# Optimization experiments

Hardware: AMD Instinct MI355X
Metric: run time of the kernel (lower is better)

The kernel has to match this reference:

```python
import jax, jax.numpy as jnp
import numpy as np

B, T, N = 128, 1024, 64


def setup_inputs() -> dict:
    key = jax.random.key(0)
    k1, k2, k3, k4, k5 = jax.random.split(key, 5)
    potentials = jax.random.normal(k1, (B, T, N), dtype=jnp.float32)
    tags = jax.random.randint(k2, (B, T), 0, N, dtype=jnp.int32)
    # valid lengths in [T//2, T] so every sequence has at least one step
    sequence_length = jax.random.randint(k3, (B,), T // 2, T + 1, dtype=jnp.int32)
    chain_kernel = jax.random.normal(k4, (N, N), dtype=jnp.float32)
    sample_weight = jax.random.uniform(k5, (B,), dtype=jnp.float32)
    return {
        "potentials": potentials,
        "tags": tags,
        "sequence_length": sequence_length,
        "chain_kernel": chain_kernel,
        "sample_weight": sample_weight,
    }


def _crf_sequence_score(potentials, tags, sequence_length, chain_kernel):
    # potentials: [B,T,N], tags: [B,T] int, chain_kernel: [N,N]
    Bx, Tx, Nx = potentials.shape
    t_idx = jnp.arange(Tx)
    mask = (t_idx[None, :] < sequence_length[:, None]).astype(potentials.dtype)  # [B,T]
    # unary score: potentials at the gold tag per step
    unary = jnp.take_along_axis(potentials, tags[..., None].astype(jnp.int32), axis=2)[..., 0]  # [B,T]
    unary_score = jnp.sum(unary * mask, axis=1)  # [B]
    # binary score: transitions tag[t] -> tag[t+1], valid if t+1 < seq_len
    trans_sc = chain_kernel[tags[:, :-1], tags[:, 1:]]  # [B,T-1]
    binary_score = jnp.sum(trans_sc * mask[:, 1:], axis=1)  # [B]
    return unary_score + binary_score


def _crf_log_norm(potentials, sequence_length, chain_kernel):
    # forward algorithm with lax.scan over time
    Bx, Tx, Nx = potentials.shape
    alpha0 = potentials[:, 0]  # [B,N]
    pots_rest = jnp.transpose(potentials[:, 1:], (1, 0, 2))  # [T-1,B,N]
    step_mask = (jnp.arange(1, Tx)[:, None] < sequence_length[None, :])  # [T-1,B]

    def step(alpha, inp):
        pot_t, m_t = inp  # [B,N], [B]
        # logsumexp over previous tag: alpha[b,i] + trans[i,j]
        new = jax.nn.logsumexp(alpha[:, :, None] + chain_kernel[None], axis=1) + pot_t
        alpha = jnp.where(m_t[:, None], new, alpha)
        return alpha, None

    alpha_T, _ = jax.lax.scan(step, alpha0, (pots_rest, step_mask))
    return jax.nn.logsumexp(alpha_T, axis=1)  # [B]


def reference(potentials, tags, sequence_length, chain_kernel, sample_weight):
    seq_score = _crf_sequence_score(potentials, tags, sequence_length, chain_kernel)
    log_norm = _crf_log_norm(potentials, sequence_length, chain_kernel)
    log_likelihood = seq_score - log_norm  # [B]
    crf_loss = -log_likelihood * sample_weight
    return jnp.mean(crf_loss)
```

## Files before the change

kernel.cpp:

```cpp
#include <hip/hip_runtime.h>
#include <math.h>

#define BB 128
#define TT 1024
#define NN 64
#define NCH 16
#define SCH 64
#define NSCORE 64
#define NSC (BB * NCH * 2)

typedef __attribute__((ext_vector_type(4))) float f32x4;
typedef __attribute__((ext_vector_type(4))) short bf16x4;

__device__ __forceinline__ float wave_sum64(float v) {
#pragma unroll
  for (int o = 32; o > 0; o >>= 1) v += __shfl_xor(v, o, 64);
  return v;
}

__device__ __forceinline__ unsigned pkbf(float lo, float hi) {
  unsigned a = __float_as_uint(lo) + 0x8000u;
  unsigned b = __float_as_uint(hi) + 0x8000u;
  return __builtin_amdgcn_perm(b, a, 0x07060302u);
}

__device__ __forceinline__ int fexp(float x) {
  unsigned u = __float_as_uint(x);
  int e = (int)((u >> 23) & 0xffu) - 127;
  if ((u & 0x7f800000u) == 0) e = 0;
  return e;
}

__global__ __launch_bounds__(128, 4) void crf_phase1(
    const float* __restrict__ pot, const int* __restrict__ tags,
    const int* __restrict__ seqlen, const float* __restrict__ K,
    unsigned* __restrict__ Hg, int* __restrict__ Eexp, float* __restrict__ score,
    float* __restrict__ accf, unsigned* __restrict__ cnt) {
  __shared__ __align__(16) unsigned sht[2][544];
  const int tid = threadIdx.x;
  const int wv = tid >> 6;
  const int lane = tid & 63;
  const int blk = blockIdx.x;

  if (blk == 0 && tid == 0) { *accf = 0.0f; *cnt = 0u; }

  if (blk < NSCORE) {
    const int b = blk * 2 + wv;
    const int L = seqlen[b];
    const int* tg = tags + b * TT;
    const float* pbase = pot + (size_t)b * TT * NN;
    float acc = 0.0f;
    for (int t = lane; t < TT; t += 64) {
      if (t < L) {
        int cc = tg[t];
        float u = pbase[(size_t)t * 64 + cc];
        float tr = (t >= 1) ? K[tg[t - 1] * 64 + cc] : 0.0f;
        acc += u + tr;
      }
    }
    acc = wave_sum64(acc);
    if (lane == 0) score[b] = acc;
    return;
  }

  const int idx = blk - NSCORE;
  const int c = idx >> 8;
  const int b = (idx >> 1) & (BB - 1);
  const int g = ((idx & 1) << 1) | wv;
  const int L = seqlen[b];
  const int q = lane >> 4, lm = lane & 15;

  const int t0 = c * SCH + 1;
  const int tend = (L < TT) ? L : TT;
  int nsteps = tend - t0;
  if (nsteps > SCH) nsteps = SCH;

  unsigned* Hc = Hg + (size_t)(b * NCH + c) * 2048 + g * 8 * 64;
  if (nsteps <= 0) {
#pragma unroll
    for (int w = 0; w < 8; w++) {
      int c0 = g * 16 + 2 * w;
      unsigned v = (lane == c0 ? 0x3F80u : 0u) | (lane == c0 + 1 ? 0x3F800000u : 0u);
      Hc[w * 64 + lane] = v;
    }
    if (lane == 0) Eexp[(b * NCH + c) * 4 + g] = 0;
    return;
  }

  bf16x4 Af[4][4];
#pragma unroll
  for (int mt = 0; mt < 4; mt++)
#pragma unroll
    for (int kt = 0; kt < 4; kt++) {
      float v0 = __expf(K[(kt * 16 + q * 4 + 0) * 64 + mt * 16 + lm]);
      float v1 = __expf(K[(kt * 16 + q * 4 + 1) * 64 + mt * 16 + lm]);
      float v2 = __expf(K[(kt * 16 + q * 4 + 2) * 64 + mt * 16 + lm]);
      float v3 = __expf(K[(kt * 16 + q * 4 + 3) * 64 + mt * 16 + lm]);
      uint2 u; u.x = pkbf(v0, v1); u.y = pkbf(v2, v3);
      Af[mt][kt] = *(bf16x4*)&u;
    }

  f32x4 D[4];
#pragma unroll
  for (int mt = 0; mt < 4; mt++) {
    f32x4 d;
#pragma unroll
    for (int r = 0; r < 4; r++)
      d[r] = __expf(K[(g * 16 + lm) * 64 + mt * 16 + q * 4 + r]);
    D[mt] = d;
  }

  const float* P = pot + (size_t)b * TT * NN + q * 4;
  f32x4 raw[4], px[4];
#pragma unroll
  for (int kt = 0; kt < 4; kt++) raw[kt] = *(const f32x4*)(P + (size_t)t0 * NN + kt * 16);
#pragma unroll
  for (int kt = 0; kt < 4; kt++) {
#pragma unroll
    for (int i = 0; i < 4; i++) px[kt][i] = __expf(raw[kt][i]);
  }
  {
    int t1 = t0 + 1 > TT - 1 ? TT - 1 : t0 + 1;
#pragma unroll
    for (int kt = 0; kt < 4; kt++) raw[kt] = *(const f32x4*)(P + (size_t)t1 * NN + kt * 16);
  }
  int etot = 0;

  for (int s = 0; s < nsteps - 1; s++) {
    float psc = 1.0f;
    if ((s & 7) == 7) {
      float d00 = __int_as_float(__builtin_amdgcn_readfirstlane(__float_as_int(D[0][0])));
      int e = fexp(d00);
      psc = ldexpf(1.0f, -e);
      etot += e;
    }
    bf16x4 Bf[4];
#pragma unroll
    for (int kt = 0; kt < 4; kt++) {
      f32x4 pv = px[kt];
      float s0 = pv[0] * psc, s1 = pv[1] * psc, s2 = pv[2] * psc, s3 = pv[3] * psc;
      f32x4 d = D[kt];
      uint2 u;
      u.x = pkbf(d[0] * s0, d[1] * s1);
      u.y = pkbf(d[2] * s2, d[3] * s3);
      Bf[kt] = *(bf16x4*)&u;
    }
#pragma unroll
    for (int kt = 0; kt < 4; kt++) {
#pragma unroll
      for (int i = 0; i < 4; i++) px[kt][i] = __expf(raw[kt][i]);
    }
    {
      int tn = t0 + s + 2; tn = tn > TT - 1 ? TT - 1 : tn;
#pragma unroll
      for (int kt = 0; kt < 4; kt++) raw[kt] = *(const f32x4*)(P + (size_t)tn * NN + kt * 16);
    }
#pragma unroll
    for (int mt = 0; mt < 4; mt++) {
      f32x4 acc = {0.f, 0.f, 0.f, 0.f};
#pragma unroll
      for (int kt = 0; kt < 4; kt++)
        acc = __builtin_amdgcn_mfma_f32_16x16x16bf16_1k(Af[mt][kt], Bf[kt], acc, 0, 0, 0);
      D[mt] = acc;
    }
  }

  {
    float hf = __int_as_float(
        __builtin_amdgcn_readfirstlane(__float_as_int(D[0][0] * px[0][0])));
    int ef = fexp(hf);
    float sc = ldexpf(1.0f, -ef);
    etot += ef;
    unsigned* sw = sht[wv];
#pragma unroll
    for (int mt = 0; mt < 4; mt++) {
      f32x4 d = D[mt]; f32x4 pv = px[mt];
      int base = lm * 33 + mt * 8 + q * 2;
      sw[base]     = pkbf(d[0] * pv[0] * sc, d[1] * pv[1] * sc);
      sw[base + 1] = pkbf(d[2] * pv[2] * sc, d[3] * pv[3] * sc);
    }
#pragma unroll
    for (int w = 0; w < 8; w++) {
      unsigned short a0 = ((const unsigned short*)(sw + (2 * w) * 33 + (lane >> 1)))[lane & 1];
      unsigned short a1 = ((const unsigned short*)(sw + (2 * w + 1) * 33 + (lane >> 1)))[lane & 1];
      Hc[w * 64 + lane] = (unsigned)a0 | ((unsigned)a1 << 16);
    }
    if (lane == 0) Eexp[(b * NCH + c) * 4 + g] = etot;
  }
}

__global__ __launch_bounds__(256, 2) void crf_phase2(
    const float* __restrict__ pot, const unsigned* __restrict__ Hg,
    const int* __restrict__ Eexp, const float* __restrict__ score,
    const float* __restrict__ wgt, float* __restrict__ accf,
    unsigned* __restrict__ cnt, float* __restrict__ out) {
  __shared__ __align__(16) float sha[64];
  __shared__ float part[4][64];
  __shared__ int shE[64];
  const int tid = threadIdx.x;
  const int w = tid >> 6;
  const int j = tid & 63;
  const int b = blockIdx.x;

  if (w == 0) {
    sha[j] = __expf(pot[(size_t)b * TT * NN + j]);
    shE[j] = Eexp[b * 64 + j];
  }
  const unsigned* Hb = Hg + (size_t)b * NCH * 2048 + (size_t)w * 8 * 64;
  unsigned rw[8], nx[8];
#pragma unroll
  for (int k = 0; k < 8; k++) rw[k] = Hb[k * 64 + j];
  __syncthreads();

  int atot = 0;
  float a = 0.0f;
  for (int c = 0; c < NCH; c++) {
    if (c + 1 < NCH) {
#pragma unroll
      for (int k = 0; k < 8; k++) nx[k] = Hb[(size_t)(c + 1) * 2048 + k * 64 + j];
    }
    float S = 0.0f;
#pragma unroll
    for (int k = 0; k < 8; k++) {
      float aLo = sha[16 * w + 2 * k], aHi = sha[16 * w + 2 * k + 1];
      S += __uint_as_float(rw[k] << 16) * aLo +
           __uint_as_float(rw[k] & 0xffff0000u) * aHi;
    }
    part[w][j] = S;
    __syncthreads();
    if (w == 0) {
      int e0 = shE[c * 4 + 0], e1 = shE[c * 4 + 1];
      int e2 = shE[c * 4 + 2], e3 = shE[c * 4 + 3];
      int em = max(max(e0, e1), max(e2, e3));
      float Sc = ldexpf(part[0][j], e0 - em) + ldexpf(part[1][j], e1 - em) +
                 ldexpf(part[2][j], e2 - em) + ldexpf(part[3][j], e3 - em);
      int er = fexp(__int_as_float(
          __builtin_amdgcn_readfirstlane(__float_as_int(Sc))));
      a = ldexpf(Sc, -er);
      sha[j] = a;
      atot += em + er;
    }
    __syncthreads();
#pragma unroll
    for (int k = 0; k < 8; k++) rw[k] = nx[k];
  }

  if (w == 0) {
    float ssum = wave_sum64(a);
    if (j == 0) {
      float lognorm = __logf(ssum) + (float)atot * 0.69314718055994530942f;
      float loss = -(score[b] - lognorm) * wgt[b];
      atomicAdd(accf, loss * (1.0f / BB));
      __threadfence();
      unsigned old = atomicAdd(cnt, 1u);
      if (old == BB - 1) out[0] = atomicAdd(accf, 0.0f);
    }
  }
}

__global__ __launch_bounds__(64) void crf_main_fb(
    const float* __restrict__ pot, const int* __restrict__ tags,
    const int* __restrict__ seqlen, const float* __restrict__ K,
    float* __restrict__ ws) {
  __shared__ float sh[4096];
  const int lane = threadIdx.x;
  const int blk = blockIdx.x;
  if (blk < BB) {
    const int b = blk;
    const int L = seqlen[b];
    float Ec[64];
#pragma unroll
    for (int i = 0; i < 64; i++) Ec[i] = __expf(K[i * 64 + lane]);
    const float* pb = pot + (size_t)b * TT * NN + lane;
    float av = __expf(pb[0]);
    int etot = 0;
    sh[lane] = av;
    float pf[8];
#pragma unroll
    for (int k = 0; k < 8; k++) pf[k] = pb[(size_t)(1 + k) * 64];
    for (int t0 = 1; t0 < L; t0 += 8) {
#pragma unroll
      for (int k = 0; k < 8; k++) {
        const int t = t0 + k;
        const float pe = __expf(pf[k]);
        int tn = t + 8; tn = tn > (TT - 1) ? (TT - 1) : tn;
        pf[k] = pb[(size_t)tn * 64];
        const float4* arow = (const float4*)(sh + ((t - 1) & 1) * 64);
        float s[8];
#pragma unroll
        for (int qq = 0; qq < 8; qq++) s[qq] = 0.0f;
#pragma unroll
        for (int qq = 0; qq < 16; qq++) {
          float4 a4 = arow[qq];
          float pr = fmaf(a4.x, Ec[4 * qq + 0], fmaf(a4.y, Ec[4 * qq + 1],
                     fmaf(a4.z, Ec[4 * qq + 2], a4.w * Ec[4 * qq + 3])));
          s[qq & 7] += pr;
        }
        float S = ((s[0] + s[1]) + (s[2] + s[3])) + ((s[4] + s[5]) + (s[6] + s[7]));
        if (t < L) {
          av = S * pe;
          if ((t & 3) == 0) {
            float m0 = __shfl(av, 0, 64);
            int e = ((__float_as_int(m0) >> 23) & 0xff) - 126;
            av = ldexpf(av, -e);
            etot += e;
          }
        }
        sh[(t & 1) * 64 + lane] = av;
      }
    }
    float ssum = wave_sum64(av);
    if (lane == 0) ws[b] = __logf(ssum) + (float)etot * 0.69314718055994530942f;
  } else {
    const int b = blk - BB;
    const int L = seqlen[b];
    for (int i = lane; i < 4096; i += 64) sh[i] = K[i];
    __syncthreads();
    const int* tg = tags + b * TT;
    const float* pbase = pot + (size_t)b * TT * NN;
    float acc = 0.0f;
    for (int t = lane; t < TT; t += 64) {
      if (t < L) {
        int cc = tg[t];
        float u = pbase[(size_t)t * 64 + cc];
        float tr = 0.0f;
        if (t >= 1) tr = sh[tg[t - 1] * 64 + cc];
        acc += u + tr;
      }
    }
    acc = wave_sum64(acc);
    if (lane == 0) ws[BB + b] = acc;
  }
}

__global__ __launch_bounds__(128) void crf_combine_fb(
    const float* __restrict__ ws, const float* __restrict__ wgt,
    float* __restrict__ out) {
  const int i = threadIdx.x;
  float lv = -(ws[BB + i] - ws[i]) * wgt[i];
  lv = wave_sum64(lv);
  __shared__ float p[2];
  if ((i & 63) == 0) p[i >> 6] = lv;
  __syncthreads();
  if (i == 0) out[0] = (p[0] + p[1]) * (1.0f / 128.0f);
}

extern "C" void kernel_launch(void* const* d_in, const int* in_sizes, int n_in,
                              void* d_out, int out_size, void* d_ws, size_t ws_size,
                              hipStream_t stream) {
  const float* pot    = (const float*)d_in[0];
  const int*   tags   = (const int*)d_in[1];
  const int*   seqlen = (const int*)d_in[2];
  const float* K      = (const float*)d_in[3];
  const float* wgt    = (const float*)d_in[4];

  const size_t HG_DW = (size_t)BB * NCH * 2048;
  const size_t NEXP  = (size_t)BB * NCH * 4;
  const size_t need  = (HG_DW + NEXP + BB + 2) * 4;

  if (ws_size >= need) {
    unsigned* Hg    = (unsigned*)d_ws;
    int* Eexp       = (int*)(Hg + HG_DW);
    float* score    = (float*)(Eexp + NEXP);
    float* accf     = score + BB;
    unsigned* cntp  = (unsigned*)(accf + 1);
    crf_phase1<<<NSC + NSCORE, 128, 0, stream>>>(pot, tags, seqlen, K, Hg, Eexp,
                                                 score, accf, cntp);
    crf_phase2<<<BB, 256, 0, stream>>>(pot, Hg, Eexp, score, wgt, accf, cntp,
                                       (float*)d_out);
  } else {
    float* ws = (float*)d_ws;
    crf_main_fb<<<256, 64, 0, stream>>>(pot, tags, seqlen, K, ws);
    crf_combine_fb<<<1, 128, 0, stream>>>(ws, wgt, (float*)d_out);
  }
}
```

Measured before the change: 185.7 us.

## Use single-wave blocks, LDS ring for exp potentials, single-wave phase2 combine

Phase1 now launches one wave per block, one per (batch, chunk, row-group). Each lane loads and exponentiates a single potential per step into a 4-deep LDS ring, instead of every lane doing 16 loads and exps. The periodic rescale is applied to the staged vector and the loop is unrolled by two. Phase2 becomes a single wave that holds two chunks of transfer matrices in registers and drops all block barriers, at the cost of much higher register pressure (64 dwords of buffers).

```diff
diff --git a/kernel.cpp b/kernel.cpp
--- a/kernel.cpp
+++ b/kernel.cpp
@@ -6,8 +6,6 @@
 #define NN 64
 #define NCH 16
 #define SCH 64
-#define NSCORE 64
-#define NSC (BB * NCH * 2)
 
 typedef __attribute__((ext_vector_type(4))) float f32x4;
 typedef __attribute__((ext_vector_type(4))) short bf16x4;
@@ -31,21 +29,20 @@
   return e;
 }
 
-__global__ __launch_bounds__(128, 4) void crf_phase1(
+__global__ __launch_bounds__(64, 4) void crf_phase1(
     const float* __restrict__ pot, const int* __restrict__ tags,
     const int* __restrict__ seqlen, const float* __restrict__ K,
     unsigned* __restrict__ Hg, int* __restrict__ Eexp, float* __restrict__ score,
     float* __restrict__ accf, unsigned* __restrict__ cnt) {
-  __shared__ __align__(16) unsigned sht[2][544];
-  const int tid = threadIdx.x;
-  const int wv = tid >> 6;
-  const int lane = tid & 63;
+  __shared__ __align__(16) float ring[4 * 64];
+  __shared__ __align__(16) unsigned sht[544];
+  const int lane = threadIdx.x;
   const int blk = blockIdx.x;
 
-  if (blk == 0 && tid == 0) { *accf = 0.0f; *cnt = 0u; }
-
-  if (blk < NSCORE) {
-    const int b = blk * 2 + wv;
+  if (blk == 0 && lane == 0) { *accf = 0.0f; *cnt = 0u; }
+
+  if (blk < BB) {
+    const int b = blk;
     const int L = seqlen[b];
     const int* tg = tags + b * TT;
     const float* pbase = pot + (size_t)b * TT * NN;
@@ -63,12 +60,13 @@
     return;
   }
 
-  const int idx = blk - NSCORE;
-  const int c = idx >> 8;
-  const int b = (idx >> 1) & (BB - 1);
-  const int g = ((idx & 1) << 1) | wv;
+  const int idx = blk - BB;
+  const int c = idx >> 9;
+  const int b = (idx >> 2) & (BB - 1);
+  const int g = idx & 3;
   const int L = seqlen[b];
   const int q = lane >> 4, lm = lane & 15;
+  const int rb = q * 4;
 
   const int t0 = c * SCH + 1;
   const int tend = (L < TT) ? L : TT;
@@ -92,10 +90,10 @@
   for (int mt = 0; mt < 4; mt++)
 #pragma unroll
     for (int kt = 0; kt < 4; kt++) {
-      float v0 = __expf(K[(kt * 16 + q * 4 + 0) * 64 + mt * 16 + lm]);
-      float v1 = __expf(K[(kt * 16 + q * 4 + 1) * 64 + mt * 16 + lm]);
-      float v2 = __expf(K[(kt * 16 + q * 4 + 2) * 64 + mt * 16 + lm]);
-      float v3 = __expf(K[(kt * 16 + q * 4 + 3) * 64 + mt * 16 + lm]);
+      float v0 = __expf(K[(kt * 16 + rb + 0) * 64 + mt * 16 + lm]);
+      float v1 = __expf(K[(kt * 16 + rb + 1) * 64 + mt * 16 + lm]);
+      float v2 = __expf(K[(kt * 16 + rb + 2) * 64 + mt * 16 + lm]);
+      float v3 = __expf(K[(kt * 16 + rb + 3) * 64 + mt * 16 + lm]);
       uint2 u; u.x = pkbf(v0, v1); u.y = pkbf(v2, v3);
       Af[mt][kt] = *(bf16x4*)&u;
     }
@@ -106,54 +104,54 @@
     f32x4 d;
 #pragma unroll
     for (int r = 0; r < 4; r++)
-      d[r] = __expf(K[(g * 16 + lm) * 64 + mt * 16 + q * 4 + r]);
+      d[r] = __expf(K[(g * 16 + lm) * 64 + mt * 16 + rb + r]);
     D[mt] = d;
   }
 
-  const float* P = pot + (size_t)b * TT * NN + q * 4;
-  f32x4 raw[4], px[4];
-#pragma unroll
-  for (int kt = 0; kt < 4; kt++) raw[kt] = *(const f32x4*)(P + (size_t)t0 * NN + kt * 16);
-#pragma unroll
-  for (int kt = 0; kt < 4; kt++) {
-#pragma unroll
-    for (int i = 0; i < 4; i++) px[kt][i] = __expf(raw[kt][i]);
-  }
-  {
-    int t1 = t0 + 1 > TT - 1 ? TT - 1 : t0 + 1;
-#pragma unroll
-    for (int kt = 0; kt < 4; kt++) raw[kt] = *(const f32x4*)(P + (size_t)t1 * NN + kt * 16);
-  }
+  const float* Pj = pot + (size_t)b * TT * NN + lane;
+#pragma unroll
+  for (int k = 0; k < 3; k++) {
+    int tt = t0 + k; tt = tt > TT - 1 ? TT - 1 : tt;
+    ring[k * 64 + lane] = __expf(Pj[(size_t)tt * NN]);
+  }
+  int t3 = t0 + 3 > TT - 1 ? TT - 1 : t0 + 3;
+  int t4 = t0 + 4 > TT - 1 ? TT - 1 : t0 + 4;
+  float rawq0 = Pj[(size_t)t3 * NN];
+  float rawq1 = Pj[(size_t)t4 * NN];
+
+  f32x4 pxc[4], pxn[4];
+#pragma unroll
+  for (int kt = 0; kt < 4; kt++)
+    pxc[kt] = *(const f32x4*)&ring[0 * 64 + kt * 16 + rb];
+
   int etot = 0;
-
+#pragma unroll 2
   for (int s = 0; s < nsteps - 1; s++) {
-    float psc = 1.0f;
     if ((s & 7) == 7) {
       float d00 = __int_as_float(__builtin_amdgcn_readfirstlane(__float_as_int(D[0][0])));
       int e = fexp(d00);
-      psc = ldexpf(1.0f, -e);
+      float psc = ldexpf(1.0f, -e);
       etot += e;
+#pragma unroll
+      for (int kt = 0; kt < 4; kt++) pxc[kt] *= psc;
     }
     bf16x4 Bf[4];
 #pragma unroll
     for (int kt = 0; kt < 4; kt++) {
-      f32x4 pv = px[kt];
-      float s0 = pv[0] * psc, s1 = pv[1] * psc, s2 = pv[2] * psc, s3 = pv[3] * psc;
-      f32x4 d = D[kt];
+      f32x4 pr = D[kt] * pxc[kt];
       uint2 u;
-      u.x = pkbf(d[0] * s0, d[1] * s1);
-      u.y = pkbf(d[2] * s2, d[3] * s3);
+      u.x = pkbf(pr[0], pr[1]);
+      u.y = pkbf(pr[2], pr[3]);
       Bf[kt] = *(bf16x4*)&u;
     }
 #pragma unroll
-    for (int kt = 0; kt < 4; kt++) {
-#pragma unroll
-      for (int i = 0; i < 4; i++) px[kt][i] = __expf(raw[kt][i]);
-    }
+    for (int kt = 0; kt < 4; kt++)
+      pxn[kt] = *(const f32x4*)&ring[((s + 1) & 3) * 64 + kt * 16 + rb];
+    ring[((s + 3) & 3) * 64 + lane] = __expf(rawq0);
+    rawq0 = rawq1;
     {
-      int tn = t0 + s + 2; tn = tn > TT - 1 ? TT - 1 : tn;
-#pragma unroll
-      for (int kt = 0; kt < 4; kt++) raw[kt] = *(const f32x4*)(P + (size_t)tn * NN + kt * 16);
+      int tn = t0 + s + 5; tn = tn > TT - 1 ? TT - 1 : tn;
+      rawq1 = Pj[(size_t)tn * NN];
     }
 #pragma unroll
     for (int mt = 0; mt < 4; mt++) {
@@ -163,98 +161,95 @@
         acc = __builtin_amdgcn_mfma_f32_16x16x16bf16_1k(Af[mt][kt], Bf[kt], acc, 0, 0, 0);
       D[mt] = acc;
     }
+#pragma unroll
+    for (int kt = 0; kt < 4; kt++) pxc[kt] = pxn[kt];
   }
 
   {
     float hf = __int_as_float(
-        __builtin_amdgcn_readfirstlane(__float_as_int(D[0][0] * px[0][0])));
+        __builtin_amdgcn_readfirstlane(__float_as_int(D[0][0] * pxc[0][0])));
     int ef = fexp(hf);
     float sc = ldexpf(1.0f, -ef);
     etot += ef;
-    unsigned* sw = sht[wv];
 #pragma unroll
     for (int mt = 0; mt < 4; mt++) {
-      f32x4 d = D[mt]; f32x4 pv = px[mt];
+      f32x4 d = D[mt]; f32x4 pv = pxc[mt];
       int base = lm * 33 + mt * 8 + q * 2;
-      sw[base]     = pkbf(d[0] * pv[0] * sc, d[1] * pv[1] * sc);
-      sw[base + 1] = pkbf(d[2] * pv[2] * sc, d[3] * pv[3] * sc);
+      sht[base]     = pkbf(d[0] * pv[0] * sc, d[1] * pv[1] * sc);
+      sht[base + 1] = pkbf(d[2] * pv[2] * sc, d[3] * pv[3] * sc);
     }
 #pragma unroll
     for (int w = 0; w < 8; w++) {
-      unsigned short a0 = ((const unsigned short*)(sw + (2 * w) * 33 + (lane >> 1)))[lane & 1];
-      unsigned short a1 = ((const unsigned short*)(sw + (2 * w + 1) * 33 + (lane >> 1)))[lane & 1];
+      unsigned short a0 = ((const unsigned short*)(sht + (2 * w) * 33 + (lane >> 1)))[lane & 1];
+      unsigned short a1 = ((const unsigned short*)(sht + (2 * w + 1) * 33 + (lane >> 1)))[lane & 1];
       Hc[w * 64 + lane] = (unsigned)a0 | ((unsigned)a1 << 16);
     }
     if (lane == 0) Eexp[(b * NCH + c) * 4 + g] = etot;
   }
 }
 
-__global__ __launch_bounds__(256, 2) void crf_phase2(
+__global__ __launch_bounds__(64, 4) void crf_phase2(
     const float* __restrict__ pot, const unsigned* __restrict__ Hg,
     const int* __restrict__ Eexp, const float* __restrict__ score,
     const float* __restrict__ wgt, float* __restrict__ accf,
     unsigned* __restrict__ cnt, float* __restrict__ out) {
   __shared__ __align__(16) float sha[64];
-  __shared__ float part[4][64];
-  __shared__ int shE[64];
-  const int tid = threadIdx.x;
-  const int w = tid >> 6;
-  const int j = tid & 63;
+  const int j = threadIdx.x;
   const int b = blockIdx.x;
 
-  if (w == 0) {
-    sha[j] = __expf(pot[(size_t)b * TT * NN + j]);
-    shE[j] = Eexp[b * 64 + j];
-  }
-  const unsigned* Hb = Hg + (size_t)b * NCH * 2048 + (size_t)w * 8 * 64;
-  unsigned rw[8], nx[8];
-#pragma unroll
-  for (int k = 0; k < 8; k++) rw[k] = Hb[k * 64 + j];
-  __syncthreads();
-
+  float a = __expf(pot[(size_t)b * TT * NN + j]);
+  sha[j] = a;
   int atot = 0;
-  float a = 0.0f;
-  for (int c = 0; c < NCH; c++) {
-    if (c + 1 < NCH) {
-#pragma unroll
-      for (int k = 0; k < 8; k++) nx[k] = Hb[(size_t)(c + 1) * 2048 + k * 64 + j];
-    }
-    float S = 0.0f;
-#pragma unroll
-    for (int k = 0; k < 8; k++) {
-      float aLo = sha[16 * w + 2 * k], aHi = sha[16 * w + 2 * k + 1];
-      S += __uint_as_float(rw[k] << 16) * aLo +
-           __uint_as_float(rw[k] & 0xffff0000u) * aHi;
-    }
-    part[w][j] = S;
-    __syncthreads();
-    if (w == 0) {
-      int e0 = shE[c * 4 + 0], e1 = shE[c * 4 + 1];
-      int e2 = shE[c * 4 + 2], e3 = shE[c * 4 + 3];
+
+  const unsigned* Hb = Hg + (size_t)b * NCH * 2048;
+  unsigned bufA[32], bufB[32];
+#pragma unroll
+  for (int k = 0; k < 32; k++) bufA[k] = Hb[k * 64 + j];
+#pragma unroll
+  for (int k = 0; k < 32; k++) bufB[k] = Hb[2048 + k * 64 + j];
+
+#pragma unroll
+  for (int cc = 0; cc < NCH; cc += 2) {
+#pragma unroll
+    for (int half = 0; half < 2; half++) {
+      const int c = cc + half;
+      unsigned* cur = half ? bufB : bufA;
+      float S[4] = {0.f, 0.f, 0.f, 0.f};
+#pragma unroll
+      for (int w4 = 0; w4 < 16; w4++) {
+        f32x4 av = *(const f32x4*)&sha[w4 * 4];
+        unsigned r0 = cur[2 * w4], r1 = cur[2 * w4 + 1];
+        S[w4 >> 2] += __uint_as_float(r0 << 16) * av[0] +
+                      __uint_as_float(r0 & 0xffff0000u) * av[1] +
+                      __uint_as_float(r1 << 16) * av[2] +
+                      __uint_as_float(r1 & 0xffff0000u) * av[3];
+      }
+      const int eb = b * 64 + c * 4;
+      int e0 = Eexp[eb + 0], e1 = Eexp[eb + 1], e2 = Eexp[eb + 2], e3 = Eexp[eb + 3];
       int em = max(max(e0, e1), max(e2, e3));
-      float Sc = ldexpf(part[0][j], e0 - em) + ldexpf(part[1][j], e1 - em) +
-                 ldexpf(part[2][j], e2 - em) + ldexpf(part[3][j], e3 - em);
+      float Sc = ldexpf(S[0], e0 - em) + ldexpf(S[1], e1 - em) +
+                 ldexpf(S[2], e2 - em) + ldexpf(S[3], e3 - em);
       int er = fexp(__int_as_float(
           __builtin_amdgcn_readfirstlane(__float_as_int(Sc))));
       a = ldexpf(Sc, -er);
+      atot += em + er;
       sha[j] = a;
-      atot += em + er;
-    }
-    __syncthreads();
-#pragma unroll
-    for (int k = 0; k < 8; k++) rw[k] = nx[k];
-  }
-
-  if (w == 0) {
-    float ssum = wave_sum64(a);
-    if (j == 0) {
-      float lognorm = __logf(ssum) + (float)atot * 0.69314718055994530942f;
-      float loss = -(score[b] - lognorm) * wgt[b];
-      atomicAdd(accf, loss * (1.0f / BB));
-      __threadfence();
-      unsigned old = atomicAdd(cnt, 1u);
-      if (old == BB - 1) out[0] = atomicAdd(accf, 0.0f);
-    }
+      if (c + 2 < NCH) {
+        const unsigned* Hn = Hb + (size_t)(c + 2) * 2048;
+#pragma unroll
+        for (int k = 0; k < 32; k++) cur[k] = Hn[k * 64 + j];
+      }
+    }
+  }
+
+  float ssum = wave_sum64(a);
+  if (j == 0) {
+    float lognorm = __logf(ssum) + (float)atot * 0.69314718055994530942f;
+    float loss = -(score[b] - lognorm) * wgt[b];
+    atomicAdd(accf, loss * (1.0f / BB));
+    __threadfence();
+    unsigned old = atomicAdd(cnt, 1u);
+    if (old == BB - 1) out[0] = atomicAdd(accf, 0.0f);
   }
 }
 
@@ -364,10 +359,10 @@
     float* score    = (float*)(Eexp + NEXP);
     float* accf     = score + BB;
     unsigned* cntp  = (unsigned*)(accf + 1);
-    crf_phase1<<<NSC + NSCORE, 128, 0, stream>>>(pot, tags, seqlen, K, Hg, Eexp,
-                                                 score, accf, cntp);
-    crf_phase2<<<BB, 256, 0, stream>>>(pot, Hg, Eexp, score, wgt, accf, cntp,
-                                       (float*)d_out);
+    crf_phase1<<<BB + BB * NCH * 4, 64, 0, stream>>>(pot, tags, seqlen, K, Hg, Eexp,
+                                                     score, accf, cntp);
+    crf_phase2<<<BB, 64, 0, stream>>>(pot, Hg, Eexp, score, wgt, accf, cntp,
+                                      (float*)d_out);
   } else {
     float* ws = (float*)d_ws;
     crf_main_fb<<<256, 64, 0, stream>>>(pot, tags, seqlen, K, ws);
```

After: 171.2 us. -7.8%, faster.
